# Optimization experiments

Measured on AMD Instinct MI355X. Metric: run time of the kernel, lower is better.

Reference implementation:

```python
import jax, jax.numpy as jnp
import numpy as np

N = 100000
E = 1600000
H = 8
D_IN = 128
D_HEAD = 16  # output_dim // n_heads


def setup_inputs() -> dict:
    key = jax.random.key(0)
    ks = jax.random.split(key, 8)
    x = jax.random.normal(ks[0], (N, D_IN), dtype=jnp.float32)
    W = jax.random.normal(ks[1], (H, D_IN, D_HEAD), dtype=jnp.float32) * 0.05
    a1 = jax.random.normal(ks[2], (H, D_HEAD), dtype=jnp.float32) * 0.1
    b1 = jnp.zeros((H,), dtype=jnp.float32)
    a2 = jax.random.normal(ks[3], (H, D_HEAD), dtype=jnp.float32) * 0.1
    b2 = jnp.zeros((H,), dtype=jnp.float32)
    src = jnp.sort(jax.random.randint(ks[4], (E,), 0, N)).astype(jnp.int32)
    dst = jax.random.randint(ks[5], (E,), 0, N).astype(jnp.int32)
    return {"x": x, "W": W, "a1": a1, "b1": b1, "a2": a2, "b2": b2,
            "src": src, "dst": dst}


def _gat_forward(x, W, a1, b1, a2, b2, src, dst):
    n = x.shape[0]
    # per-head linear transform: [H, N, D_HEAD]
    feats = jnp.einsum('nd,hdo->hno', x, W)
    # per-node attention scalars (1x1 conv with bias): [H, N]
    f1 = jnp.einsum('hno,ho->hn', feats, a1) + b1[:, None]
    f2 = jnp.einsum('hno,ho->hn', feats, a2) + b2[:, None]
    # edge logits: logit[e] = f1[src[e]] + f2[dst[e]]  -> [E, H]
    e = f1[:, src].T + f2[:, dst].T
    e = jnp.maximum(0.2 * e, e)  # leaky_relu
    # sparse row-softmax over each source node's neighbors (segment softmax)
    m = jax.ops.segment_max(e, src, num_segments=n)           # [N, H]
    ex = jnp.exp(e - m[src])                                   # [E, H]
    denom = jax.ops.segment_sum(ex, src, num_segments=n)      # [N, H]
    coef = ex / denom[src]                                     # [E, H]
    # spmm: out[i] = sum_{j in N(i)} coef[ij] * feats[j]
    feats_nhd = jnp.transpose(feats, (1, 0, 2))                # [N, H, D_HEAD]
    msg = coef[:, :, None] * feats_nhd[dst]                    # [E, H, D_HEAD]
    out = jax.ops.segment_sum(msg, src, num_segments=n)       # [N, H, D_HEAD]
    out = out.reshape(n, H * D_HEAD)
    return jax.nn.elu(out)


def reference(x, W, a1, b1, a2, b2, src, dst):
    return _gat_forward(x, W, a1, b1, a2, b2, src, dst)
```

## Files before the change

### kernel.cpp

```cpp
#include <hip/hip_runtime.h>
#include <hip/hip_bf16.h>
#include <math.h>

#define HEADS 8
#define D_IN 128
#define D_HEAD 16
#define D_OUT 128

typedef unsigned short ushort_t;
typedef unsigned int uint_t;
typedef __attribute__((ext_vector_type(8))) short short8;
typedef __attribute__((ext_vector_type(4))) float floatx4;

static __device__ inline uint_t f32_to_bf16(float f) {
    uint_t u = __float_as_uint(f);
    return (u + 0x7fffu + ((u >> 16) & 1u)) >> 16;
}
static __device__ inline uint_t pack_bf16(float lo, float hi) {
    return (f32_to_bf16(hi) << 16) | f32_to_bf16(lo);
}
static __device__ inline float bf_lo(uint_t p) { return __uint_as_float(p << 16); }
static __device__ inline float bf_hi(uint_t p) { return __uint_as_float(p & 0xffff0000u); }

#define PREP_WBLOCKS 64
__global__ __launch_bounds__(256) void prep_kernel(
    const float* __restrict__ Wg,
    const float* __restrict__ a1, const float* __restrict__ a2,
    ushort_t* __restrict__ Wfrag,
    const int* __restrict__ src, int* __restrict__ row_ptr, int n, int e)
{
    const int rp_blocks = (e + 1 + 255) / 256;
    const int bid = blockIdx.x;
    if (bid < PREP_WBLOCKS) {
        int t = bid * 256 + threadIdx.x;
        int j    = t & 7;
        int lane = (t >> 3) & 63;
        int ks   = (t >> 9) & 3;
        int ct   = t >> 11;
        int k = ks * 32 + (lane >> 4) * 8 + j;
        int m = lane & 15;
        float v = Wg[(size_t)ct * (D_IN * D_HEAD) + k * D_HEAD + m];
        Wfrag[t] = (ushort_t)f32_to_bf16(v);
    } else if (bid < PREP_WBLOCKS + rp_blocks) {
        int i = (bid - PREP_WBLOCKS) * 256 + threadIdx.x;
        if (i > e) return;
        int sp = (i == 0) ? -1 : src[i - 1];
        int sc = (i == e) ? n  : src[i];
        for (int node = sp + 1; node <= sc; ++node) row_ptr[node] = i;
    } else {
#pragma unroll
        for (int i = 0; i < 8; ++i) {
            int t = i * 256 + threadIdx.x;
            int j  = t & 7;
            int ln = (t >> 3) & 63;
            int ks = (t >> 9) & 3;
            int k  = ks * 32 + (ln >> 4) * 8 + j;
            int mm = ln & 15;
            int h  = mm & 7;
            const float* wrow = Wg + (size_t)h * (D_IN * D_HEAD) + k * D_HEAD;
            const float* av   = (mm < 8 ? a1 : a2) + h * D_HEAD;
            float s = 0.f;
#pragma unroll
            for (int o = 0; o < D_HEAD; ++o) s = fmaf(wrow[o], av[o], s);
            Wfrag[8 * 2048 + t] = (ushort_t)f32_to_bf16(s);
        }
    }
}

__global__ __launch_bounds__(256) void gemm_feats_mfma(
    const float* __restrict__ x, const ushort_t* __restrict__ Wfrag,
    const float* __restrict__ b1, const float* __restrict__ b2,
    ushort_t* __restrict__ feats, float* __restrict__ f1,
    float* __restrict__ f2, int n)
{
    __shared__ ushort_t Xs[64][136];
    __shared__ ushort_t WsF[9 * 2048];

    const int tid  = threadIdx.x;
    const int wave = tid >> 6;
    const int lane = tid & 63;
    const int row0 = blockIdx.x * 64;

    {
        const uint4* wsrc = (const uint4*)Wfrag;
        uint4*       wdst = (uint4*)WsF;
#pragma unroll
        for (int i = 0; i < 9; ++i) wdst[i * 256 + tid] = wsrc[i * 256 + tid];
    }
#pragma unroll
    for (int it = 0; it < 8; ++it) {
        int idx = it * 256 + tid;
        int r   = idx >> 5;
        int c4  = (idx & 31) * 4;
        float4 v = make_float4(0.f, 0.f, 0.f, 0.f);
        if (row0 + r < n) v = *(const float4*)(x + (size_t)(row0 + r) * D_IN + c4);
        *(uint2*)&Xs[r][c4] = make_uint2(pack_bf16(v.x, v.y), pack_bf16(v.z, v.w));
    }
    __syncthreads();

    const int m  = lane & 15;
    const int kg = lane >> 4;

    floatx4 acc[9];
#pragma unroll
    for (int ct = 0; ct < 9; ++ct) acc[ct] = (floatx4){0.f, 0.f, 0.f, 0.f};

#pragma unroll
    for (int ks = 0; ks < 4; ++ks) {
        short8 xb = *(const short8*)&Xs[wave * 16 + m][ks * 32 + kg * 8];
#pragma unroll
        for (int ct = 0; ct < 9; ++ct) {
            short8 wa = *(const short8*)&WsF[((ct * 4 + ks) * 64 + lane) * 8];
            acc[ct] = __builtin_amdgcn_mfma_f32_16x16x32_bf16(wa, xb, acc[ct], 0, 0, 0);
        }
    }

    const int node = row0 + wave * 16 + m;
    if (node < n) {
#pragma unroll
        for (int ct = 0; ct < 8; ++ct) {
            uint_t lo = pack_bf16(acc[ct][0], acc[ct][1]);
            uint_t hi = pack_bf16(acc[ct][2], acc[ct][3]);
            *(uint2*)(feats + (size_t)node * D_OUT + ct * 16 + kg * 4) = make_uint2(lo, hi);
        }
        const float* bb = (kg < 2) ? b1 : b2;
        float4 bv = *(const float4*)(bb + (kg & 1) * 4);
        float4 o = make_float4(acc[8][0] + bv.x, acc[8][1] + bv.y,
                               acc[8][2] + bv.z, acc[8][3] + bv.w);
        float* dstp = ((kg < 2) ? f1 : f2) + (size_t)node * HEADS + (kg & 1) * 4;
        *(float4*)dstp = o;
    }
}

__global__ __launch_bounds__(256) void aggregate_kernel(
    const int* __restrict__ row_ptr, const int* __restrict__ dst,
    const ushort_t* __restrict__ feats,
    const float* __restrict__ f1, const float* __restrict__ f2,
    float* __restrict__ out, int n)
{
    int node = blockIdx.x * 4 + (threadIdx.x >> 6);
    node = __builtin_amdgcn_readfirstlane(node);
    if (node >= n) return;
    const int lane = threadIdx.x & 63;
    const int h = lane >> 3;

    const float f1v   = f1[(size_t)node * HEADS + h];
    const int   start = row_ptr[node];
    const int   end   = row_ptr[node + 1];

    const ushort_t* fl = feats + 2 * lane;

    float s = 0.f, ax = 0.f, ay = 0.f;
    int e = start;
    for (; e + 8 <= end; e += 8) {
        int d[8];
#pragma unroll
        for (int q = 0; q < 8; ++q) d[q] = dst[e + q];
        const int   dq = dst[e + (lane & 7)];
        const float g  = f2[(size_t)dq * HEADS + h];
        float z = f1v + g;
        z = fmaxf(z, 0.2f * z);
        const float w = __expf(z);
        uint_t p[8];
#pragma unroll
        for (int q = 0; q < 8; ++q)
            p[q] = *(const uint_t*)(fl + (size_t)d[q] * D_OUT);
#pragma unroll
        for (int q = 0; q < 8; ++q) {
            const float wq = __shfl(w, (lane & 56) | q);
            s += wq;
            ax = fmaf(wq, bf_lo(p[q]), ax);
            ay = fmaf(wq, bf_hi(p[q]), ay);
        }
    }
    for (; e < end; ++e) {
        const int d = dst[e];
        const float g = f2[(size_t)d * HEADS + h];
        const uint_t p = *(const uint_t*)(fl + (size_t)d * D_OUT);
        float z = f1v + g;
        z = fmaxf(z, 0.2f * z);
        const float w = __expf(z);
        s += w;
        ax = fmaf(w, bf_lo(p), ax);
        ay = fmaf(w, bf_hi(p), ay);
    }

    float rx = 0.f, ry = 0.f;
    if (end > start) {
        rx = ax / s;
        ry = ay / s;
        rx = rx > 0.f ? rx : expm1f(rx);
        ry = ry > 0.f ? ry : expm1f(ry);
    }
    *(float2*)(out + (size_t)node * D_OUT + 2 * lane) = make_float2(rx, ry);
}

extern "C" void kernel_launch(void* const* d_in, const int* in_sizes, int n_in,
                              void* d_out, int out_size, void* d_ws, size_t ws_size,
                              hipStream_t stream)
{
    const float* x  = (const float*)d_in[0];
    const float* W  = (const float*)d_in[1];
    const float* a1 = (const float*)d_in[2];
    const float* b1 = (const float*)d_in[3];
    const float* a2 = (const float*)d_in[4];
    const float* b2 = (const float*)d_in[5];
    const int* src  = (const int*)d_in[6];
    const int* dst  = (const int*)d_in[7];
    float* out = (float*)d_out;

    const int n = in_sizes[0] / D_IN;
    const int e = in_sizes[6];

    char* ws = (char*)d_ws;
    size_t off = 0;
    ushort_t* feats = (ushort_t*)(ws + off);
    off += (size_t)n * D_OUT * sizeof(ushort_t); off = (off + 255) & ~(size_t)255;
    float* f1 = (float*)(ws + off);
    off += (size_t)n * HEADS * sizeof(float);    off = (off + 255) & ~(size_t)255;
    float* f2 = (float*)(ws + off);
    off += (size_t)n * HEADS * sizeof(float);    off = (off + 255) & ~(size_t)255;
    int* row_ptr = (int*)(ws + off);
    off += (size_t)(n + 1) * sizeof(int);        off = (off + 255) & ~(size_t)255;
    ushort_t* Wfrag = (ushort_t*)(ws + off);

    dim3 blk(256);
    const int rp_blocks = (e + 1 + 255) / 256;
    prep_kernel<<<dim3(PREP_WBLOCKS + rp_blocks + 1), blk, 0, stream>>>(
        W, a1, a2, Wfrag, src, row_ptr, n, e);
    gemm_feats_mfma<<<dim3((n + 63) / 64), blk, 0, stream>>>(
        x, Wfrag, b1, b2, feats, f1, f2, n);
    aggregate_kernel<<<dim3((n + 3) / 4), blk, 0, stream>>>(
        row_ptr, dst, feats, f1, f2, out, n);
}
```

Before: 217.8 us.

## Restructure aggregation into 16-edge half-wave batches and drop LDS staging in GEMM

The aggregation kernel now handles 16 edges per iteration, with padded indices instead of a scalar tail loop. Each half-wave gathers alternate edges with 8-byte loads of four features per lane, and the two halves are combined with a cross-half shuffle reduction. The feature GEMM drops shared-memory staging of x and W: it loads x straight from global into MFMA fragments and reads W fragments from global or cache. Float-to-bf16 packing uses the hardware v_cvt_pk_bf16_f32 instruction. The aim is fewer loop iterations, more memory-level parallelism in the gather and less LDS and barrier overhead, at the cost of repeated global W reads and some wasted work on padded edges.

Result: slower. 271.4 us (+24.6%).

```diff
diff --git a/kernel.cpp b/kernel.cpp
--- a/kernel.cpp
+++ b/kernel.cpp
@@ -1,5 +1,4 @@
 #include <hip/hip_runtime.h>
-#include <hip/hip_bf16.h>
 #include <math.h>
 
 #define HEADS 8
@@ -18,6 +17,11 @@
 }
 static __device__ inline uint_t pack_bf16(float lo, float hi) {
     return (f32_to_bf16(hi) << 16) | f32_to_bf16(lo);
+}
+static __device__ inline uint_t cvtpk_bf16(float lo, float hi) {
+    uint_t r;
+    asm("v_cvt_pk_bf16_f32 %0, %1, %2" : "=v"(r) : "v"(lo), "v"(hi));
+    return r;
 }
 static __device__ inline float bf_lo(uint_t p) { return __uint_as_float(p << 16); }
 static __device__ inline float bf_hi(uint_t p) { return __uint_as_float(p & 0xffff0000u); }
@@ -73,54 +77,45 @@
     ushort_t* __restrict__ feats, float* __restrict__ f1,
     float* __restrict__ f2, int n)
 {
-    __shared__ ushort_t Xs[64][136];
-    __shared__ ushort_t WsF[9 * 2048];
-
     const int tid  = threadIdx.x;
     const int wave = tid >> 6;
     const int lane = tid & 63;
-    const int row0 = blockIdx.x * 64;
-
-    {
-        const uint4* wsrc = (const uint4*)Wfrag;
-        uint4*       wdst = (uint4*)WsF;
-#pragma unroll
-        for (int i = 0; i < 9; ++i) wdst[i * 256 + tid] = wsrc[i * 256 + tid];
-    }
-#pragma unroll
-    for (int it = 0; it < 8; ++it) {
-        int idx = it * 256 + tid;
-        int r   = idx >> 5;
-        int c4  = (idx & 31) * 4;
-        float4 v = make_float4(0.f, 0.f, 0.f, 0.f);
-        if (row0 + r < n) v = *(const float4*)(x + (size_t)(row0 + r) * D_IN + c4);
-        *(uint2*)&Xs[r][c4] = make_uint2(pack_bf16(v.x, v.y), pack_bf16(v.z, v.w));
-    }
-    __syncthreads();
-
-    const int m  = lane & 15;
-    const int kg = lane >> 4;
+    const int m    = lane & 15;
+    const int kg   = lane >> 4;
+    const int node = blockIdx.x * 64 + wave * 16 + m;
+    const bool valid = node < n;
 
     floatx4 acc[9];
 #pragma unroll
     for (int ct = 0; ct < 9; ++ct) acc[ct] = (floatx4){0.f, 0.f, 0.f, 0.f};
 
+    const float* xp = x + (size_t)(valid ? node : 0) * D_IN + kg * 8;
+
 #pragma unroll
     for (int ks = 0; ks < 4; ++ks) {
-        short8 xb = *(const short8*)&Xs[wave * 16 + m][ks * 32 + kg * 8];
+        float4 va = make_float4(0.f, 0.f, 0.f, 0.f), vb = va;
+        if (valid) {
+            va = *(const float4*)(xp + ks * 32);
+            vb = *(const float4*)(xp + ks * 32 + 4);
+        }
+        union { uint_t u[4]; short8 s8; } cv;
+        cv.u[0] = cvtpk_bf16(va.x, va.y);
+        cv.u[1] = cvtpk_bf16(va.z, va.w);
+        cv.u[2] = cvtpk_bf16(vb.x, vb.y);
+        cv.u[3] = cvtpk_bf16(vb.z, vb.w);
+        const short8 xb = cv.s8;
 #pragma unroll
         for (int ct = 0; ct < 9; ++ct) {
-            short8 wa = *(const short8*)&WsF[((ct * 4 + ks) * 64 + lane) * 8];
+            short8 wa = *(const short8*)(Wfrag + ((size_t)(ct * 4 + ks) * 64 + lane) * 8);
             acc[ct] = __builtin_amdgcn_mfma_f32_16x16x32_bf16(wa, xb, acc[ct], 0, 0, 0);
         }
     }
 
-    const int node = row0 + wave * 16 + m;
-    if (node < n) {
+    if (valid) {
 #pragma unroll
         for (int ct = 0; ct < 8; ++ct) {
-            uint_t lo = pack_bf16(acc[ct][0], acc[ct][1]);
-            uint_t hi = pack_bf16(acc[ct][2], acc[ct][3]);
+            uint_t lo = cvtpk_bf16(acc[ct][0], acc[ct][1]);
+            uint_t hi = cvtpk_bf16(acc[ct][2], acc[ct][3]);
             *(uint2*)(feats + (size_t)node * D_OUT + ct * 16 + kg * 4) = make_uint2(lo, hi);
         }
         const float* bb = (kg < 2) ? b1 : b2;
@@ -142,57 +137,66 @@
     node = __builtin_amdgcn_readfirstlane(node);
     if (node >= n) return;
     const int lane = threadIdx.x & 63;
-    const int h = lane >> 3;
-
-    const float f1v   = f1[(size_t)node * HEADS + h];
-    const int   start = row_ptr[node];
-    const int   end   = row_ptr[node + 1];
-
-    const ushort_t* fl = feats + 2 * lane;
-
-    float s = 0.f, ax = 0.f, ay = 0.f;
-    int e = start;
-    for (; e + 8 <= end; e += 8) {
-        int d[8];
-#pragma unroll
-        for (int q = 0; q < 8; ++q) d[q] = dst[e + q];
-        const int   dq = dst[e + (lane & 7)];
-        const float g  = f2[(size_t)dq * HEADS + h];
-        float z = f1v + g;
-        z = fmaxf(z, 0.2f * z);
-        const float w = __expf(z);
-        uint_t p[8];
-#pragma unroll
-        for (int q = 0; q < 8; ++q)
-            p[q] = *(const uint_t*)(fl + (size_t)d[q] * D_OUT);
-#pragma unroll
-        for (int q = 0; q < 8; ++q) {
-            const float wq = __shfl(w, (lane & 56) | q);
-            s += wq;
-            ax = fmaf(wq, bf_lo(p[q]), ax);
-            ay = fmaf(wq, bf_hi(p[q]), ay);
-        }
-    }
-    for (; e < end; ++e) {
-        const int d = dst[e];
-        const float g = f2[(size_t)d * HEADS + h];
-        const uint_t p = *(const uint_t*)(fl + (size_t)d * D_OUT);
-        float z = f1v + g;
-        z = fmaxf(z, 0.2f * z);
-        const float w = __expf(z);
-        s += w;
-        ax = fmaf(w, bf_lo(p), ax);
-        ay = fmaf(w, bf_hi(p), ay);
-    }
-
-    float rx = 0.f, ry = 0.f;
-    if (end > start) {
-        rx = ax / s;
-        ry = ay / s;
-        rx = rx > 0.f ? rx : expm1f(rx);
-        ry = ry > 0.f ? ry : expm1f(ry);
-    }
-    *(float2*)(out + (size_t)node * D_OUT + 2 * lane) = make_float2(rx, ry);
+    const int h  = lane >> 3;
+    const int q  = lane & 7;
+    const int hf    = lane >> 5;
+    const int sl    = lane & 31;
+    const int sbase = (sl >> 2) * 8 + hf;
+
+    const float f1v  = f1[(size_t)node * HEADS + h];
+    const int  start = row_ptr[node];
+    const int  end   = row_ptr[node + 1];
+
+    float s = 0.f, c0 = 0.f, c1 = 0.f, c2 = 0.f, c3 = 0.f;
+
+    for (int e = start; e < end; e += 16) {
+        int d[16];
+#pragma unroll
+        for (int t = 0; t < 16; ++t) {
+            int ee = e + t;
+            d[t] = dst[ee < end ? ee : end - 1];
+        }
+        const int ea = e + q, eb = e + 8 + q;
+        const int da = dst[ea < end ? ea : end - 1];
+        const int db = dst[eb < end ? eb : end - 1];
+        float za = f1v + f2[(size_t)da * HEADS + h];
+        float zb = f1v + f2[(size_t)db * HEADS + h];
+        za = fmaxf(za, 0.2f * za);
+        zb = fmaxf(zb, 0.2f * zb);
+        const float wa = (ea < end) ? __expf(za) : 0.f;
+        const float wb = (eb < end) ? __expf(zb) : 0.f;
+
+#pragma unroll
+        for (int p = 0; p < 8; ++p) {
+            const int row = hf ? d[2 * p + 1] : d[2 * p];
+            const uint2 pr = *(const uint2*)(feats + (size_t)row * D_OUT + 4 * sl);
+            const float w = __shfl(p < 4 ? wa : wb, sbase + ((2 * p) & 7));
+            s  += w;
+            c0 = fmaf(w, bf_lo(pr.x), c0);
+            c1 = fmaf(w, bf_hi(pr.x), c1);
+            c2 = fmaf(w, bf_lo(pr.y), c2);
+            c3 = fmaf(w, bf_hi(pr.y), c3);
+        }
+    }
+
+    s  += __shfl_xor(s, 32);
+    c0 += __shfl_xor(c0, 32);
+    c1 += __shfl_xor(c1, 32);
+    c2 += __shfl_xor(c2, 32);
+    c3 += __shfl_xor(c3, 32);
+
+    if (lane < 32) {
+        float4 r = make_float4(0.f, 0.f, 0.f, 0.f);
+        if (end > start) {
+            const float inv = 1.f / s;
+            r.x = c0 * inv; r.y = c1 * inv; r.z = c2 * inv; r.w = c3 * inv;
+            r.x = r.x > 0.f ? r.x : expm1f(r.x);
+            r.y = r.y > 0.f ? r.y : expm1f(r.y);
+            r.z = r.z > 0.f ? r.z : expm1f(r.z);
+            r.w = r.w > 0.f ? r.w : expm1f(r.w);
+        }
+        *(float4*)(out + (size_t)node * D_OUT + 4 * sl) = r;
+    }
 }
 
 extern "C" void kernel_launch(void* const* d_in, const int* in_sizes, int n_in,
```
